# Performance work log

Measured on AMD Instinct MI355X. Metric: run time of the kernel, lower is better.

Reference implementation:

```python
import jax, jax.numpy as jnp
import numpy as np

V, E, S, NCLASS = 50000, 512, 1024, 2
B, L = 64, 256


def setup_inputs() -> dict:
    key = jax.random.key(0)
    ks = jax.random.split(key, 8)
    inputs = jax.random.randint(ks[0], (B, L), 0, V)
    emb_table = jax.random.normal(ks[1], (V, E), dtype=jnp.float32) * 0.02
    Wc = jax.random.normal(ks[2], (S, 2 * E), dtype=jnp.float32) * (1.0 / np.sqrt(2 * E))
    bc = jnp.zeros((S,), dtype=jnp.float32)
    W1 = jax.random.normal(ks[3], (50, S), dtype=jnp.float32) * (1.0 / np.sqrt(S))
    b1 = jnp.zeros((50,), dtype=jnp.float32)
    W2 = jax.random.normal(ks[4], (NCLASS, 50), dtype=jnp.float32) * (1.0 / np.sqrt(50))
    b2 = jnp.zeros((NCLASS,), dtype=jnp.float32)
    return {"inputs": inputs, "emb_table": emb_table, "Wc": Wc, "bc": bc,
            "W1": W1, "b1": b1, "W2": W2, "b2": b2}


def reference(inputs, emb_table, Wc, bc, W1, b1, W2, b2):
    # [B, L, E] embedding lookup
    w_embs = emb_table[inputs]
    # sliding-window pair concat: [B, L-1, 2E]
    pairs = jnp.concatenate([w_embs[:, :-1, :], w_embs[:, 1:, :]], axis=-1)
    # conv linear: [B, L-1, S]
    conv = jnp.einsum('blf,sf->bls', pairs, Wc) + bc
    # max-pool over positions then sigmoid: [B, S]
    sent = jax.nn.sigmoid(jnp.max(conv, axis=1))
    # classifier: S -> 50 -> NCLASS
    h = jnp.einsum('bs,hs->bh', sent, W1) + b1
    logits = jnp.einsum('bh,ch->bc', h, W2) + b2
    out = jax.nn.log_softmax(logits, axis=1)
    return jnp.squeeze(out, axis=1) if out.shape[1] == 1 else out
```

## Files before the change

kernel.cpp:

```cpp
#include <hip/hip_runtime.h>

#define VV 50000
#define EE 512
#define SS 1024
#define BB 64
#define LL 256
#define NTOK (BB*LL)
#define XROWS_PAD (NTOK + 8)

#define SCALE_A 0x79797979
#define SCALE_B 0x7A7A7A7A

typedef __attribute__((ext_vector_type(8))) int i32x8;
typedef __attribute__((ext_vector_type(4))) float f32x4;

static __device__ __forceinline__ void glds16(const void* g, void* l) {
    __builtin_amdgcn_global_load_lds(
        (const __attribute__((address_space(1))) unsigned int*)g,
        (__attribute__((address_space(3))) unsigned int*)l,
        16, 0, 0);
}

static __device__ __forceinline__ uint2 pack8_fp8(float4 v0, float4 v1, float s) {
    int r0 = __builtin_amdgcn_cvt_pk_fp8_f32(v0.x * s, v0.y * s, 0, 0);
    r0 = __builtin_amdgcn_cvt_pk_fp8_f32(v0.z * s, v0.w * s, r0, 1);
    int r1 = __builtin_amdgcn_cvt_pk_fp8_f32(v1.x * s, v1.y * s, 0, 0);
    r1 = __builtin_amdgcn_cvt_pk_fp8_f32(v1.z * s, v1.w * s, r1, 1);
    uint2 o; o.x = (unsigned)r0; o.y = (unsigned)r1; return o;
}

static __device__ __forceinline__ i32x8 ldfrag(const unsigned char* rowbase, int c0, int c1) {
    const uint4 lo = *(const uint4*)(rowbase + c0 * 16);
    const uint4 hi = *(const uint4*)(rowbase + c1 * 16);
    i32x8 f;
    f[0] = lo.x; f[1] = lo.y; f[2] = lo.z; f[3] = lo.w;
    f[4] = hi.x; f[5] = hi.y; f[6] = hi.z; f[7] = hi.w;
    return f;
}

__global__ __launch_bounds__(256)
void prep_kernel(const int* __restrict__ inputs,
                 const float* __restrict__ emb,
                 const float* __restrict__ Wc,
                 unsigned char* __restrict__ Xq,
                 unsigned char* __restrict__ Wq,
                 unsigned int* __restrict__ pre) {
    const int tid = threadIdx.x;
    if (blockIdx.x < 4096) {
        const int t = blockIdx.x * 4 + (tid >> 6);
        const int lane = tid & 63;
        const int idx = inputs[t];
        const float* src = emb + (size_t)idx * EE + lane * 8;
        const float4 v0 = *(const float4*)src;
        const float4 v1 = *(const float4*)(src + 4);
        *(uint2*)(Xq + (size_t)t * EE + lane * 8) = pack8_fp8(v0, v1, 64.0f);
    } else {
        const int bb = blockIdx.x - 4096;
        const int i = (bb * 256 + tid) * 8;
        const float4 v0 = *(const float4*)(Wc + i);
        const float4 v1 = *(const float4*)(Wc + i + 4);
        *(uint2*)(Wq + i) = pack8_fp8(v0, v1, 32.0f);
        if (bb < BB) {
            uint4 z = {0u, 0u, 0u, 0u};
            *(uint4*)(pre + bb * SS + tid * 4) = z;
        }
    }
}

__global__ __launch_bounds__(256, 3)
void conv_gemm_kernel(const unsigned char* __restrict__ Xq,
                      const unsigned char* __restrict__ Wq,
                      unsigned int* __restrict__ pre) {
    __shared__ unsigned char sX[136 * 128];
    __shared__ unsigned char sW[256 * 128];

    const int tid = threadIdx.x;
    const int w = tid >> 6;
    const int lane = tid & 63;
    const int wx = w & 1;
    const int wy = w >> 1;
    const int m0 = blockIdx.y * 128;
    const int s0 = blockIdx.x * 128;

    f32x4 acc[4][4];
    #pragma unroll
    for (int mt = 0; mt < 4; ++mt)
        #pragma unroll
        for (int nt = 0; nt < 4; ++nt)
            acc[mt][nt] = (f32x4){0.f, 0.f, 0.f, 0.f};

    const int lrow = lane >> 3;
    const int lcolsw = (((lane & 7) ^ lrow) * 16);
    const int quad = lane >> 4;
    const int l15 = lane & 15;
    const int swA  = l15 & 7;
    const int swA1 = (l15 + 1) & 7;
    const int cb0 = 2 * quad;

    const unsigned char* pA  = sX + (wy * 64 + l15) * 128;
    const unsigned char* pA1 = sX + (wy * 64 + l15 + 1) * 128;
    const unsigned char* pB1 = sW + (wx * 64 + l15) * 128;
    const unsigned char* pB2 = sW + (128 + wx * 64 + l15) * 128;
    const int cA0 = cb0 ^ swA,  cA1 = (cb0 + 1) ^ swA;
    const int cS0 = cb0 ^ swA1, cS1 = (cb0 + 1) ^ swA1;

    for (int kt = 0; kt < 4; ++kt) {
        const int k0 = kt * 128;
        #pragma unroll
        for (int i = 0; i < 4; ++i) {
            const int c = w + 4 * i;
            glds16(Xq + (size_t)(m0 + c * 8 + lrow) * EE + k0 + lcolsw,
                   (char*)sX + c * 1024);
        }
        if (w == 0) {
            glds16(Xq + (size_t)(m0 + 128 + lrow) * EE + k0 + lcolsw,
                   (char*)sX + 16 * 1024);
        }
        #pragma unroll
        for (int i = 0; i < 8; ++i) {
            const int c = w + 4 * i;
            const int wrow = c * 8 + lrow;
            const int h = wrow >> 7, sl = wrow & 127;
            glds16(Wq + (size_t)(s0 + sl) * 1024 + h * 512 + k0 + lcolsw,
                   (char*)sW + c * 1024);
        }
        __syncthreads();

        i32x8 aA[4], aB[4];
        #pragma unroll
        for (int mt = 0; mt < 4; ++mt) {
            aA[mt] = ldfrag(pA  + mt * 2048, cA0, cA1);
            aB[mt] = ldfrag(pA1 + mt * 2048, cS0, cS1);
        }
        #pragma unroll
        for (int nt = 0; nt < 4; ++nt) {
            const i32x8 b1 = ldfrag(pB1 + nt * 2048, cA0, cA1);
            const i32x8 b2 = ldfrag(pB2 + nt * 2048, cA0, cA1);
            #pragma unroll
            for (int mt = 0; mt < 4; ++mt)
                acc[mt][nt] = __builtin_amdgcn_mfma_scale_f32_16x16x128_f8f6f4(
                    aA[mt], b1, acc[mt][nt], 0, 0, 0, SCALE_A, 0, SCALE_B);
            #pragma unroll
            for (int mt = 0; mt < 4; ++mt)
                acc[mt][nt] = __builtin_amdgcn_mfma_scale_f32_16x16x128_f8f6f4(
                    aB[mt], b2, acc[mt][nt], 0, 0, 0, SCALE_A, 0, SCALE_B);
        }
        __syncthreads();
    }

    const int b = m0 >> 8;
    float* smax = (float*)sX;
    #pragma unroll
    for (int nt = 0; nt < 4; ++nt) {
        float cmax = -3.4e38f;
        #pragma unroll
        for (int mt = 0; mt < 4; ++mt) {
            const int rbase = m0 + wy * 64 + mt * 16 + quad * 4;
            #pragma unroll
            for (int r = 0; r < 4; ++r) {
                const float v = acc[mt][nt][r];
                const bool valid = (((rbase + r) & 255) != 255);
                cmax = valid ? fmaxf(cmax, v) : cmax;
            }
        }
        cmax = fmaxf(cmax, __shfl_xor(cmax, 16));
        cmax = fmaxf(cmax, __shfl_xor(cmax, 32));
        if (lane < 16) smax[wy * 128 + wx * 64 + nt * 16 + lane] = cmax;
    }
    __syncthreads();
    if (tid < 128) {
        const float m = fmaxf(smax[tid], smax[128 + tid]);
        const unsigned int u = __float_as_uint(m);
        const unsigned int e = (u & 0x80000000u) ? ~u : (u | 0x80000000u);
        atomicMax(pre + b * SS + s0 + tid, e);
    }
}

__global__ __launch_bounds__(1024)
void classifier_kernel(const unsigned int* __restrict__ pre,
                       const float* __restrict__ bc,
                       const float* __restrict__ W1,
                       const float* __restrict__ b1,
                       const float* __restrict__ W2,
                       const float* __restrict__ b2,
                       float* __restrict__ out) {
    __shared__ float ssig[SS];
    __shared__ float sh[64];
    const int b = blockIdx.x;
    const int tid = threadIdx.x;
    {
        const unsigned int e = pre[b * SS + tid];
        const unsigned int u = (e & 0x80000000u) ? (e & 0x7FFFFFFFu) : ~e;
        const float x = __uint_as_float(u) + bc[tid];
        ssig[tid] = 1.0f / (1.0f + __expf(-x));
    }
    if (tid >= 50 && tid < 64) sh[tid] = 0.f;
    __syncthreads();
    const int w = tid >> 6, lane = tid & 63;
    const float4* sp = (const float4*)ssig;
    for (int j = w; j < 50; j += 16) {
        const float4* wp = (const float4*)(W1 + j * SS);
        float p = 0.f;
        #pragma unroll
        for (int i = 0; i < 4; ++i) {
            const float4 a = sp[lane + i * 64];
            const float4 g = wp[lane + i * 64];
            p += a.x * g.x + a.y * g.y + a.z * g.z + a.w * g.w;
        }
        #pragma unroll
        for (int off = 32; off; off >>= 1) p += __shfl_xor(p, off);
        if (lane == 0) sh[j] = p + b1[j];
    }
    __syncthreads();
    if (w == 0) {
        const float hj = (lane < 50) ? sh[lane] : 0.f;
        const float w2a = (lane < 50) ? W2[lane] : 0.f;
        const float w2b = (lane < 50) ? W2[50 + lane] : 0.f;
        float l0 = hj * w2a, l1 = hj * w2b;
        #pragma unroll
        for (int off = 32; off; off >>= 1) {
            l0 += __shfl_xor(l0, off);
            l1 += __shfl_xor(l1, off);
        }
        if (lane == 0) {
            l0 += b2[0]; l1 += b2[1];
            const float m = fmaxf(l0, l1);
            const float lse = m + logf(expf(l0 - m) + expf(l1 - m));
            out[b * 2 + 0] = l0 - lse;
            out[b * 2 + 1] = l1 - lse;
        }
    }
}

extern "C" void kernel_launch(void* const* d_in, const int* in_sizes, int n_in,
                              void* d_out, int out_size, void* d_ws, size_t ws_size,
                              hipStream_t stream) {
    const int*   inputs = (const int*)  d_in[0];
    const float* emb    = (const float*)d_in[1];
    const float* Wc     = (const float*)d_in[2];
    const float* bc     = (const float*)d_in[3];
    const float* W1     = (const float*)d_in[4];
    const float* b1     = (const float*)d_in[5];
    const float* W2     = (const float*)d_in[6];
    const float* b2     = (const float*)d_in[7];
    float* out = (float*)d_out;

    unsigned char* Xq = (unsigned char*)d_ws;
    unsigned char* Wq = Xq + (size_t)XROWS_PAD * EE;
    unsigned int*  pre = (unsigned int*)(Wq + (size_t)SS * 1024);

    prep_kernel<<<4608, 256, 0, stream>>>(inputs, emb, Wc, Xq, Wq, pre);
    dim3 grid(SS / 128, NTOK / 128);
    conv_gemm_kernel<<<grid, 256, 0, stream>>>(Xq, Wq, pre);
    classifier_kernel<<<BB, 1024, 0, stream>>>(pre, bc, W1, b1, W2, b2, out);
}
```

Before: 203.4 us.

## Tile conv GEMM per full sequence with 32x32 MFMA and drop atomics

Each conv GEMM block now covers a whole 256-token sequence (256x128 tile) and uses 32x32x64 scaled FP8 MFMAs instead of 16x16x128. Because one block owns all positions of a batch row, the max-pool result is written directly as a float, which removes the atomicMax, the order-preserving float encoding and the zero-init of the pool buffer in the prep kernel. In exchange the block uses more LDS and registers, occupancy hint drops from 3 to 2, and the grid has half as many blocks.

After: 179.9 us (median of 2 runs). 1.13x faster.

```diff
diff --git a/kernel.cpp b/kernel.cpp
--- a/kernel.cpp
+++ b/kernel.cpp
@@ -12,7 +12,7 @@
 #define SCALE_B 0x7A7A7A7A
 
 typedef __attribute__((ext_vector_type(8))) int i32x8;
-typedef __attribute__((ext_vector_type(4))) float f32x4;
+typedef __attribute__((ext_vector_type(16))) float f32x16;
 
 static __device__ __forceinline__ void glds16(const void* g, void* l) {
     __builtin_amdgcn_global_load_lds(
@@ -43,8 +43,7 @@
                  const float* __restrict__ emb,
                  const float* __restrict__ Wc,
                  unsigned char* __restrict__ Xq,
-                 unsigned char* __restrict__ Wq,
-                 unsigned int* __restrict__ pre) {
+                 unsigned char* __restrict__ Wq) {
     const int tid = threadIdx.x;
     if (blockIdx.x < 4096) {
         const int t = blockIdx.x * 4 + (tid >> 6);
@@ -60,18 +59,14 @@
         const float4 v0 = *(const float4*)(Wc + i);
         const float4 v1 = *(const float4*)(Wc + i + 4);
         *(uint2*)(Wq + i) = pack8_fp8(v0, v1, 32.0f);
-        if (bb < BB) {
-            uint4 z = {0u, 0u, 0u, 0u};
-            *(uint4*)(pre + bb * SS + tid * 4) = z;
-        }
-    }
-}
-
-__global__ __launch_bounds__(256, 3)
+    }
+}
+
+__global__ __launch_bounds__(256, 2)
 void conv_gemm_kernel(const unsigned char* __restrict__ Xq,
                       const unsigned char* __restrict__ Wq,
-                      unsigned int* __restrict__ pre) {
-    __shared__ unsigned char sX[136 * 128];
+                      float* __restrict__ pre) {
+    __shared__ unsigned char sX[264 * 128];
     __shared__ unsigned char sW[256 * 128];
 
     const int tid = threadIdx.x;
@@ -79,105 +74,103 @@
     const int lane = tid & 63;
     const int wx = w & 1;
     const int wy = w >> 1;
-    const int m0 = blockIdx.y * 128;
+    const int b  = blockIdx.y;
+    const int m0 = b * 256;
     const int s0 = blockIdx.x * 128;
 
-    f32x4 acc[4][4];
+    f32x16 acc[4][2];
     #pragma unroll
-    for (int mt = 0; mt < 4; ++mt)
-        #pragma unroll
-        for (int nt = 0; nt < 4; ++nt)
-            acc[mt][nt] = (f32x4){0.f, 0.f, 0.f, 0.f};
+    for (int rt = 0; rt < 4; ++rt)
+        #pragma unroll
+        for (int nt = 0; nt < 2; ++nt)
+            acc[rt][nt] = (f32x16)(0.f);
 
     const int lrow = lane >> 3;
     const int lcolsw = (((lane & 7) ^ lrow) * 16);
-    const int quad = lane >> 4;
-    const int l15 = lane & 15;
-    const int swA  = l15 & 7;
-    const int swA1 = (l15 + 1) & 7;
-    const int cb0 = 2 * quad;
-
-    const unsigned char* pA  = sX + (wy * 64 + l15) * 128;
-    const unsigned char* pA1 = sX + (wy * 64 + l15 + 1) * 128;
-    const unsigned char* pB1 = sW + (wx * 64 + l15) * 128;
-    const unsigned char* pB2 = sW + (128 + wx * 64 + l15) * 128;
-    const int cA0 = cb0 ^ swA,  cA1 = (cb0 + 1) ^ swA;
-    const int cS0 = cb0 ^ swA1, cS1 = (cb0 + 1) ^ swA1;
-
+    const int l31 = lane & 31;
+    const int lh  = lane >> 5;
+    const int sz0 = lane & 7;
+    const int sz1 = (l31 + 1) & 7;
+
+    const int cb0 = 2 * lh;
+    const int cb1 = 4 + 2 * lh;
+
+    const unsigned char* pA0 = sX + (wy * 128 + l31) * 128;
+    const unsigned char* pA1 = pA0 + 128;
+    const unsigned char* pB1 = sW + (wx * 64 + l31) * 128;
+    const unsigned char* pB2 = pB1 + 128 * 128;
+
+    #pragma unroll 1
     for (int kt = 0; kt < 4; ++kt) {
         const int k0 = kt * 128;
         #pragma unroll
-        for (int i = 0; i < 4; ++i) {
-            const int c = w + 4 * i;
-            glds16(Xq + (size_t)(m0 + c * 8 + lrow) * EE + k0 + lcolsw,
-                   (char*)sX + c * 1024);
-        }
-        if (w == 0) {
-            glds16(Xq + (size_t)(m0 + 128 + lrow) * EE + k0 + lcolsw,
-                   (char*)sX + 16 * 1024);
-        }
-        #pragma unroll
         for (int i = 0; i < 8; ++i) {
-            const int c = w + 4 * i;
-            const int wrow = c * 8 + lrow;
+            const int st = w + 4 * i;
+            glds16(Xq + (size_t)(m0 + st * 8 + lrow) * EE + k0 + lcolsw,
+                   (char*)sX + st * 1024);
+            const int wrow = st * 8 + lrow;
             const int h = wrow >> 7, sl = wrow & 127;
             glds16(Wq + (size_t)(s0 + sl) * 1024 + h * 512 + k0 + lcolsw,
-                   (char*)sW + c * 1024);
+                   (char*)sW + st * 1024);
+        }
+        if (w == 0) {
+            glds16(Xq + (size_t)(m0 + 256 + lrow) * EE + k0 + lcolsw,
+                   (char*)sX + 32 * 1024);
         }
         __syncthreads();
 
-        i32x8 aA[4], aB[4];
-        #pragma unroll
-        for (int mt = 0; mt < 4; ++mt) {
-            aA[mt] = ldfrag(pA  + mt * 2048, cA0, cA1);
-            aB[mt] = ldfrag(pA1 + mt * 2048, cS0, cS1);
-        }
-        #pragma unroll
-        for (int nt = 0; nt < 4; ++nt) {
-            const i32x8 b1 = ldfrag(pB1 + nt * 2048, cA0, cA1);
-            const i32x8 b2 = ldfrag(pB2 + nt * 2048, cA0, cA1);
+        i32x8 b1[2][2], b2[2][2];
+        #pragma unroll
+        for (int nt = 0; nt < 2; ++nt) {
+            b1[nt][0] = ldfrag(pB1 + nt * 4096, cb0 ^ sz0, (cb0 + 1) ^ sz0);
+            b1[nt][1] = ldfrag(pB1 + nt * 4096, cb1 ^ sz0, (cb1 + 1) ^ sz0);
+            b2[nt][0] = ldfrag(pB2 + nt * 4096, cb0 ^ sz0, (cb0 + 1) ^ sz0);
+            b2[nt][1] = ldfrag(pB2 + nt * 4096, cb1 ^ sz0, (cb1 + 1) ^ sz0);
+        }
+        #pragma unroll
+        for (int rt = 0; rt < 4; ++rt) {
+            i32x8 a0[2], a1[2];
+            a0[0] = ldfrag(pA0 + rt * 4096, cb0 ^ sz0, (cb0 + 1) ^ sz0);
+            a0[1] = ldfrag(pA0 + rt * 4096, cb1 ^ sz0, (cb1 + 1) ^ sz0);
+            a1[0] = ldfrag(pA1 + rt * 4096, cb0 ^ sz1, (cb0 + 1) ^ sz1);
+            a1[1] = ldfrag(pA1 + rt * 4096, cb1 ^ sz1, (cb1 + 1) ^ sz1);
             #pragma unroll
-            for (int mt = 0; mt < 4; ++mt)
-                acc[mt][nt] = __builtin_amdgcn_mfma_scale_f32_16x16x128_f8f6f4(
-                    aA[mt], b1, acc[mt][nt], 0, 0, 0, SCALE_A, 0, SCALE_B);
-            #pragma unroll
-            for (int mt = 0; mt < 4; ++mt)
-                acc[mt][nt] = __builtin_amdgcn_mfma_scale_f32_16x16x128_f8f6f4(
-                    aB[mt], b2, acc[mt][nt], 0, 0, 0, SCALE_A, 0, SCALE_B);
+            for (int s = 0; s < 2; ++s)
+                #pragma unroll
+                for (int nt = 0; nt < 2; ++nt) {
+                    acc[rt][nt] = __builtin_amdgcn_mfma_scale_f32_32x32x64_f8f6f4(
+                        a0[s], b1[nt][s], acc[rt][nt], 0, 0, 0, SCALE_A, 0, SCALE_B);
+                    acc[rt][nt] = __builtin_amdgcn_mfma_scale_f32_32x32x64_f8f6f4(
+                        a1[s], b2[nt][s], acc[rt][nt], 0, 0, 0, SCALE_A, 0, SCALE_B);
+                }
         }
         __syncthreads();
     }
 
-    const int b = m0 >> 8;
     float* smax = (float*)sX;
     #pragma unroll
-    for (int nt = 0; nt < 4; ++nt) {
+    for (int nt = 0; nt < 2; ++nt) {
         float cmax = -3.4e38f;
         #pragma unroll
-        for (int mt = 0; mt < 4; ++mt) {
-            const int rbase = m0 + wy * 64 + mt * 16 + quad * 4;
+        for (int rt = 0; rt < 4; ++rt) {
             #pragma unroll
-            for (int r = 0; r < 4; ++r) {
-                const float v = acc[mt][nt][r];
-                const bool valid = (((rbase + r) & 255) != 255);
-                cmax = valid ? fmaxf(cmax, v) : cmax;
+            for (int reg = 0; reg < 16; ++reg) {
+                const int row = (reg & 3) + 8 * (reg >> 2) + 4 * lh;
+                const int tl = wy * 128 + rt * 32 + row;
+                const float v = acc[rt][nt][reg];
+                cmax = (tl != 255) ? fmaxf(cmax, v) : cmax;
             }
         }
-        cmax = fmaxf(cmax, __shfl_xor(cmax, 16));
         cmax = fmaxf(cmax, __shfl_xor(cmax, 32));
-        if (lane < 16) smax[wy * 128 + wx * 64 + nt * 16 + lane] = cmax;
+        if (lane < 32) smax[wy * 128 + wx * 64 + nt * 32 + lane] = cmax;
     }
     __syncthreads();
-    if (tid < 128) {
-        const float m = fmaxf(smax[tid], smax[128 + tid]);
-        const unsigned int u = __float_as_uint(m);
-        const unsigned int e = (u & 0x80000000u) ? ~u : (u | 0x80000000u);
-        atomicMax(pre + b * SS + s0 + tid, e);
-    }
+    if (tid < 128)
+        pre[b * SS + s0 + tid] = fmaxf(smax[tid], smax[128 + tid]);
 }
 
 __global__ __launch_bounds__(1024)
-void classifier_kernel(const unsigned int* __restrict__ pre,
+void classifier_kernel(const float* __restrict__ pre,
                        const float* __restrict__ bc,
                        const float* __restrict__ W1,
                        const float* __restrict__ b1,
@@ -189,9 +182,7 @@
     const int b = blockIdx.x;
     const int tid = threadIdx.x;
     {
-        const unsigned int e = pre[b * SS + tid];
-        const unsigned int u = (e & 0x80000000u) ? (e & 0x7FFFFFFFu) : ~e;
-        const float x = __uint_as_float(u) + bc[tid];
+        const float x = pre[b * SS + tid] + bc[tid];
         ssig[tid] = 1.0f / (1.0f + __expf(-x));
     }
     if (tid >= 50 && tid < 64) sh[tid] = 0.f;
@@ -247,10 +238,10 @@
 
     unsigned char* Xq = (unsigned char*)d_ws;
     unsigned char* Wq = Xq + (size_t)XROWS_PAD * EE;
-    unsigned int*  pre = (unsigned int*)(Wq + (size_t)SS * 1024);
-
-    prep_kernel<<<4608, 256, 0, stream>>>(inputs, emb, Wc, Xq, Wq, pre);
-    dim3 grid(SS / 128, NTOK / 128);
+    float*         pre = (float*)(Wq + (size_t)SS * 1024);
+
+    prep_kernel<<<4608, 256, 0, stream>>>(inputs, emb, Wc, Xq, Wq);
+    dim3 grid(SS / 128, NTOK / 256);
     conv_gemm_kernel<<<grid, 256, 0, stream>>>(Xq, Wq, pre);
     classifier_kernel<<<BB, 1024, 0, stream>>>(pre, bc, W1, b1, W2, b2, out);
 }
```
